# Optimization experiments

Hardware: AMD Instinct MI355X
Metric: run time of the kernel (lower is better)

The kernel has to match this reference:

```python
import jax, jax.numpy as jnp
import numpy as np

B, N, T, F, H, O = 32, 256, 64, 16, 128, 1  # batch, nodes, seq_len, input, hidden, output


def setup_inputs() -> dict:
    key = jax.random.key(0)
    ks = jax.random.split(key, 14)
    s = 0.05
    nrm = lambda k, shp: jax.random.normal(k, shp, jnp.float32) * s
    return {
        "x": jax.random.normal(ks[0], (B, N, T, F), jnp.float32),
        "A": jax.random.normal(ks[1], (N, N), jnp.float32),
        "W_ih0": nrm(ks[2], (4 * H, F)),
        "W_hh0": nrm(ks[3], (4 * H, H)),
        "b_ih0": nrm(ks[4], (4 * H,)),
        "b_hh0": nrm(ks[5], (4 * H,)),
        "W_ih1": nrm(ks[6], (4 * H, H)),
        "W_hh1": nrm(ks[7], (4 * H, H)),
        "b_ih1": nrm(ks[8], (4 * H,)),
        "b_hh1": nrm(ks[9], (4 * H,)),
        "W1": nrm(ks[10], (H, H)),
        "W2": nrm(ks[11], (H, H)),
        "W3": nrm(ks[12], (H, H)),
        "Wfc": nrm(ks[13], (O, H)),
    }


def _lstm_layer(inp, W_ih, W_hh, b_ih, b_hh):
    # inp: (BN, T, F_in). PyTorch LSTM gate order: i, f, g, o.
    BN = inp.shape[0]
    Hd = W_hh.shape[1]
    h0 = jnp.zeros((BN, Hd), inp.dtype)
    c0 = jnp.zeros((BN, Hd), inp.dtype)

    def step(carry, x_t):
        h, c = carry
        g = x_t @ W_ih.T + b_ih + h @ W_hh.T + b_hh
        i, f, gg, o = jnp.split(g, 4, axis=-1)
        c = jax.nn.sigmoid(f) * c + jax.nn.sigmoid(i) * jnp.tanh(gg)
        h = jax.nn.sigmoid(o) * jnp.tanh(c)
        return (h, c), h

    (hT, _), hs = jax.lax.scan(step, (h0, c0), jnp.swapaxes(inp, 0, 1))
    return jnp.swapaxes(hs, 0, 1), hT  # (BN, T, H), (BN, H)


def reference(x, A, W_ih0, W_hh0, b_ih0, b_hh0, W_ih1, W_hh1, b_ih1, b_hh1, W1, W2, W3, Wfc):
    Bx, Nx, Tx, Fx = x.shape
    # Batch the per-node LSTM calls: all (batch, node) pairs share LSTM weights.
    xs = x.reshape(Bx * Nx, Tx, Fx)
    h1_seq, _ = _lstm_layer(xs, W_ih0, W_hh0, b_ih0, b_hh0)
    _, hT = _lstm_layer(h1_seq, W_ih1, W_hh1, b_ih1, b_hh1)  # last layer final hidden
    h_LSTM = hT.reshape(Bx, Nx, -1).transpose(0, 2, 1)  # (B, H, N)

    A_p = jax.nn.sigmoid(A)
    HA = jnp.einsum('bhn,nl->bhl', h_LSTM, A_p)        # H @ A'
    h_A = HA.transpose(0, 2, 1)                        # (B, N, H)
    W1hA = jnp.einsum('bnh,gh->bgn', h_A, W1)          # (B, H, N)
    mid = jax.nn.relu(jnp.einsum('bnh,gh->bng', h_A, W2))
    W3r = jnp.einsum('bng,fg->bfn', mid, W3)           # (B, H, N)
    ATW = jnp.einsum('bhn,nl->bhl', W3r, A_p)
    alpha = 0.9
    h_out = (1.0 - alpha) * ATW + alpha * W1hA         # (B, H, N)
    # Per-node MLP (shared weights) + sigmoid, batched over nodes.
    out = jax.nn.sigmoid(jnp.einsum('bhn,oh->bno', h_out, Wfc))  # (B, N, O)
    return out
```

## Files before the change

### kernel.cpp

```cpp
#include <hip/hip_runtime.h>


typedef __attribute__((ext_vector_type(4))) float f32x4;
typedef __attribute__((ext_vector_type(16))) float f32x16;
typedef __attribute__((ext_vector_type(2))) float f32x2;
typedef __attribute__((ext_vector_type(8))) __bf16 bf16x8;
typedef __attribute__((ext_vector_type(8))) unsigned short u16x8;
typedef __attribute__((ext_vector_type(4))) unsigned short u16x4;

#define DEV static __device__ __forceinline__

DEV unsigned short f2bf(float f) {
  unsigned u = __builtin_bit_cast(unsigned, f);
  u = u + 0x7fffu + ((u >> 16) & 1u);
  return (unsigned short)(u >> 16);
}
DEV float bf2f(unsigned short s) {
  unsigned u = ((unsigned)s) << 16;
  return __builtin_bit_cast(float, u);
}

DEV float fexp2(float x) { return __builtin_amdgcn_exp2f(x); }
DEV f32x2 exp2v2(f32x2 x) { f32x2 r; r[0] = fexp2(x[0]); r[1] = fexp2(x[1]); return r; }
DEV f32x2 rcpv2(f32x2 x) {
  f32x2 r; r[0] = __builtin_amdgcn_rcpf(x[0]); r[1] = __builtin_amdgcn_rcpf(x[1]); return r;
}

DEV unsigned cell_pair(f32x2 gi, f32x2 gf, f32x2 gg, f32x2 go, f32x2& cs) {
  const float K2 = 2.88539008f;
  f32x2 one = {1.f, 1.f};
  f32x2 t1 = exp2v2(gg);
  f32x2 t2 = exp2v2((f32x2){-gi[0], -gi[1]});
  f32x2 ef = exp2v2((f32x2){-gf[0], -gf[1]});
  f32x2 d1 = t1 + one;
  f32x2 den1 = d1 * t2 + d1;
  f32x2 it = (t1 - one) * rcpv2(den1);
  cs = rcpv2(one + ef) * cs + (f32x2){K2 * it[0], K2 * it[1]};
  f32x2 t3 = exp2v2(cs);
  f32x2 t4 = exp2v2((f32x2){-go[0], -go[1]});
  f32x2 d3 = t3 + one;
  f32x2 den3 = d3 * t4 + d3;
  f32x2 h = (t3 - one) * rcpv2(den3);
  unsigned r;
  asm("v_cvt_pk_bf16_f32 %0, %1, %2" : "=v"(r) : "v"(h[0]), "v"(h[1]));
  return r;
}

#define O_W0PK   0
#define O_W1PK   163840
#define O_APK    425984
#define O_W1APK  557056
#define O_W2APK  589824
#define O_W3APK  622592
#define O_BIAS0  655360
#define O_BIAS1  657408
#define O_HTT    659456
#define O_HAT    2756608
#define O_MIDT   4853760
#define O_W1HAT  6950912
#define O_W3R    9048064
#define O_XPK    11145216
#define O_H1     44699648

#define PREP_TOT 328704

__global__ void prep_kernel(const float* __restrict__ A,
    const float* __restrict__ Wih0, const float* __restrict__ Whh0,
    const float* __restrict__ bih0, const float* __restrict__ bhh0,
    const float* __restrict__ Wih1, const float* __restrict__ Whh1,
    const float* __restrict__ bih1, const float* __restrict__ bhh1,
    const float* __restrict__ W1, const float* __restrict__ W2,
    const float* __restrict__ W3, char* __restrict__ ws)
{
  const float K1 = 1.44269504f, K2 = 2.88539008f;
  int idx = blockIdx.x * blockDim.x + threadIdx.x;
  if (idx >= PREP_TOT) return;
  if (idx < 81920) {
    int o = idx, i = o & 7, l = (o >> 3) & 63, f = o >> 9;
    int kt = f % 10, W = f / 10;
    int rho = l & 31, hik = l >> 5;
    int p = rho & 3, hi = (rho >> 2) & 1, q = rho >> 3;
    int gc = p * 128 + 8 * W + 4 * hi + q;
    float sc = (p == 2) ? K2 : K1;
    int k = 16 * kt + 8 * hik + i;
    float v;
    if (k < 128) v = Whh0[gc * 128 + k];
    else {
      int kk = k - 128;
      v = (kk < 16) ? Wih0[gc * 16 + kk]
                    : (kk == 16 ? (bih0[gc] + bhh0[gc]) : 0.f);
    }
    ((unsigned short*)(ws + O_W0PK))[idx] = f2bf(v * sc);
  } else if (idx < 212992) {
    int o = idx - 81920, i = o & 7, l = (o >> 3) & 63, f = o >> 9;
    int kt = f & 15, W = f >> 4;
    int rho = l & 31, hik = l >> 5;
    int p = rho & 3, hi = (rho >> 2) & 1, q = rho >> 3;
    int gc = p * 128 + 8 * W + 4 * hi + q;
    float sc = (p == 2) ? K2 : K1;
    int k = 16 * kt + 8 * hik + i;
    float v = (k < 128) ? Wih1[gc * 128 + k] : Whh1[gc * 128 + (k - 128)];
    ((unsigned short*)(ws + O_W1PK))[o] = f2bf(v * sc);
  } else if (idx < 278528) {
    int o = idx - 212992, i = o & 7, l = (o >> 3) & 63, f = o >> 9;
    int kt = f & 7, ct = f >> 3;
    int n = 32 * kt + 8 * (l >> 4) + i;
    int lc = 16 * ct + (l & 15);
    float e = fexp2(-K1 * A[n * 256 + lc]);
    ((unsigned short*)(ws + O_APK))[o] = f2bf(__builtin_amdgcn_rcpf(1.f + e));
  } else if (idx < 327680) {
    int o = idx - 278528;
    int m = o >> 14;
    int oo = o & 16383;
    int i = oo & 7, l = (oo >> 3) & 63, f = oo >> 9;
    int kt = f & 3, rt = f >> 2;
    int g = 16 * rt + (l & 15);
    int k = 32 * kt + 8 * (l >> 4) + i;
    const float* W = (m == 0) ? W1 : (m == 1) ? W2 : W3;
    unsigned short* dst = (unsigned short*)(ws + ((m == 0) ? O_W1APK : (m == 1) ? O_W2APK : O_W3APK));
    dst[oo] = f2bf(W[g * 128 + k]);
  } else if (idx < 328192) {
    int c = idx - 327680;
    ((float*)(ws + O_BIAS0))[c] = bih0[c] + bhh0[c];
  } else {
    int c = idx - 328192;
    float sc = ((c >> 7) == 2) ? K2 : K1;
    ((float*)(ws + O_BIAS1))[c] = (bih1[c] + bhh1[c]) * sc;
  }
}

__global__ void prepx_kernel(const float* __restrict__ x, char* __restrict__ ws)
{
  int tid = blockIdx.x * 256 + threadIdx.x;
  int lane = tid & 63;
  int slice = (tid >> 6) & 1;
  int t = (tid >> 7) & 63;
  int rt32 = tid >> 13;
  int col = lane & 31, hi = lane >> 5;
  u16x8 v = (u16x8)0;
  if (slice == 0) {
    const float* p = x + ((long)(rt32 * 32 + col) * 64 + t) * 16 + 8 * hi;
    float4 a = *(const float4*)p;
    float4 b = *(const float4*)(p + 4);
    v[0] = f2bf(a.x); v[1] = f2bf(a.y); v[2] = f2bf(a.z); v[3] = f2bf(a.w);
    v[4] = f2bf(b.x); v[5] = f2bf(b.y); v[6] = f2bf(b.z); v[7] = f2bf(b.w);
  } else if (hi == 0) {
    v[0] = 0x3F80;
  }
  ((u16x8*)(ws + O_XPK))[tid] = v;
}

__global__ __launch_bounds__(1024, 4) void lstm0_k(char* __restrict__ ws, int row_base)
{
  const unsigned short* W0pk = (const unsigned short*)(ws + O_W0PK);
  const unsigned short* xpk = (const unsigned short*)(ws + O_XPK);
  unsigned short* h1 = (unsigned short*)(ws + O_H1);

  int tid = threadIdx.x;
  int Wv = tid >> 6, l = tid & 63, col = l & 31, hi = l >> 5;
  int lrow = blockIdx.x * 32;
  long grow0 = (long)row_base + lrow;

  __shared__ unsigned char hlds[2][8192];
  ((unsigned long long*)hlds[0])[tid] = 0ull;

  bf16x8 Af[10];
#pragma unroll
  for (int kt = 0; kt < 10; kt++)
    Af[kt] = ((const bf16x8*)W0pk)[(Wv * 10 + kt) * 64 + l];

  f32x2 cs01 = {0.f, 0.f}, cs23 = {0.f, 0.f};

  int rd[8];
#pragma unroll
  for (int ks = 0; ks < 8; ks++)
    rd[ks] = col * 256 + ((32 * ks + 16 * hi) ^ ((col & 15) << 4));
  int whp = col * 256 + ((16 * Wv + 8 * hi) ^ ((col & 15) << 4));

  int pr = tid >> 5, pc8 = tid & 31;
  int sld = pr * 256 + ((8 * pc8) ^ ((pr & 15) << 4));
  unsigned short* st = h1 + (long)(lrow + pr) * 8192 + 4 * pc8;

  long xbase = (grow0 >> 5) * 8192 + l;
  const bf16x8* xpf = (const bf16x8*)xpk;
  bf16x8 xb0 = xpf[xbase], xb1 = xpf[xbase + 64];
  __syncthreads();

  for (int t = 0; t < 64; t++) {
    const unsigned char* rbuf = hlds[t & 1];
    unsigned char* wbuf = hlds[(t & 1) ^ 1];
    int tn = (t < 63) ? t + 1 : 63;
    bf16x8 xb0n = xpf[xbase + tn * 128];
    bf16x8 xb1n = xpf[xbase + tn * 128 + 64];

    f32x16 acc = (f32x16)0.f;
    __builtin_amdgcn_s_setprio(1);
#pragma unroll
    for (int ks = 0; ks < 8; ks++) {
      bf16x8 hb = *(const bf16x8*)(rbuf + rd[ks]);
      acc = __builtin_amdgcn_mfma_f32_32x32x16_bf16(Af[ks], hb, acc, 0, 0, 0);
    }
    acc = __builtin_amdgcn_mfma_f32_32x32x16_bf16(Af[8], xb0, acc, 0, 0, 0);
    acc = __builtin_amdgcn_mfma_f32_32x32x16_bf16(Af[9], xb1, acc, 0, 0, 0);
    __builtin_amdgcn_s_setprio(0);

    unsigned pk01 = cell_pair((f32x2){acc[0], acc[4]}, (f32x2){acc[1], acc[5]},
                              (f32x2){acc[2], acc[6]}, (f32x2){acc[3], acc[7]}, cs01);
    unsigned pk23 = cell_pair((f32x2){acc[8], acc[12]}, (f32x2){acc[9], acc[13]},
                              (f32x2){acc[10], acc[14]}, (f32x2){acc[11], acc[15]}, cs23);
    *(unsigned long long*)(wbuf + whp) =
        ((unsigned long long)pk23 << 32) | pk01;
    xb0 = xb0n; xb1 = xb1n;
    __syncthreads();
    *(unsigned long long*)(st + t * 128) =
        *(const unsigned long long*)(hlds[(t & 1) ^ 1] + sld);
  }
}

__global__ __launch_bounds__(1024, 4) void lstm1_k(char* __restrict__ ws, int row_base)
{
  const unsigned short* W1pk = (const unsigned short*)(ws + O_W1PK);
  const float* bias1 = (const float*)(ws + O_BIAS1);
  const unsigned short* h1 = (const unsigned short*)(ws + O_H1);
  unsigned short* hTt = (unsigned short*)(ws + O_HTT);

  int tid = threadIdx.x;
  int Wv = tid >> 6, l = tid & 63, col = l & 31, hi = l >> 5;
  int lrow = blockIdx.x * 32;
  long grow0 = (long)row_base + lrow;

  __shared__ unsigned char hlds[2][8192];
  __shared__ unsigned char h1s[2][8192];
  ((unsigned long long*)hlds[0])[tid] = 0ull;

  int prow = tid >> 5, pc8 = tid & 31;
  const unsigned short* s0 = h1 + (long)(lrow + prow) * 8192 + 4 * pc8;
  int d0 = prow * 256 + ((8 * pc8) ^ ((prow & 15) << 4));
  *(unsigned long long*)(h1s[0] + d0) = *(const unsigned long long*)s0;

  bf16x8 Af[16];
#pragma unroll
  for (int kt = 0; kt < 16; kt++)
    Af[kt] = ((const bf16x8*)W1pk)[(Wv * 16 + kt) * 64 + l];

  int u0 = 8 * Wv + 4 * hi;
  f32x16 bias_c;
#pragma unroll
  for (int r = 0; r < 16; r++)
    bias_c[r] = bias1[(r & 3) * 128 + u0 + (r >> 2)];

  f32x2 cs01 = {0.f, 0.f}, cs23 = {0.f, 0.f};

  int rd[8];
#pragma unroll
  for (int ks = 0; ks < 8; ks++)
    rd[ks] = col * 256 + ((32 * ks + 16 * hi) ^ ((col & 15) << 4));
  int whp = col * 256 + ((16 * Wv + 8 * hi) ^ ((col & 15) << 4));
  __syncthreads();

  for (int t = 0; t < 64; t++) {
    const unsigned char* rbuf = hlds[t & 1];
    unsigned char* wbuf = hlds[(t & 1) ^ 1];
    const unsigned char* h1r = h1s[t & 1];
    unsigned char* h1w = h1s[(t & 1) ^ 1];
    int tn = (t < 63) ? t + 1 : 63;
    unsigned long long pf = *(const unsigned long long*)(s0 + tn * 128);

    f32x16 acc = bias_c;
    __builtin_amdgcn_s_setprio(1);
#pragma unroll
    for (int ks = 0; ks < 8; ks++) {
      bf16x8 xb = *(const bf16x8*)(h1r + rd[ks]);
      acc = __builtin_amdgcn_mfma_f32_32x32x16_bf16(Af[ks], xb, acc, 0, 0, 0);
    }
#pragma unroll
    for (int ks = 0; ks < 8; ks++) {
      bf16x8 hb = *(const bf16x8*)(rbuf + rd[ks]);
      acc = __builtin_amdgcn_mfma_f32_32x32x16_bf16(Af[8 + ks], hb, acc, 0, 0, 0);
    }
    __builtin_amdgcn_s_setprio(0);

    unsigned pk01 = cell_pair((f32x2){acc[0], acc[4]}, (f32x2){acc[1], acc[5]},
                              (f32x2){acc[2], acc[6]}, (f32x2){acc[3], acc[7]}, cs01);
    unsigned pk23 = cell_pair((f32x2){acc[8], acc[12]}, (f32x2){acc[9], acc[13]},
                              (f32x2){acc[10], acc[14]}, (f32x2){acc[11], acc[15]}, cs23);
    *(unsigned long long*)(wbuf + whp) =
        ((unsigned long long)pk23 << 32) | pk01;
    *(unsigned long long*)(h1w + d0) = pf;
    __syncthreads();
  }

  {
    unsigned long long hp = *(const unsigned long long*)(hlds[0] + whp);
    long grow = grow0 + col;
    long base = ((grow >> 8) * 128) * 256 + (grow & 255);
#pragma unroll
    for (int j = 0; j < 4; j++)
      hTt[base + (long)(u0 + j) * 256] = (unsigned short)((hp >> (16 * j)) & 0xffff);
  }
}

__global__ __launch_bounds__(256, 2) void g1_kernel(char* __restrict__ ws)
{
  const unsigned short* hTt = (const unsigned short*)(ws + O_HTT);
  const unsigned short* Apk = (const unsigned short*)(ws + O_APK);
  unsigned short* HAt = (unsigned short*)(ws + O_HAT);
  int tid = threadIdx.x, w = tid >> 6, l = tid & 63, lr = l & 15, lq = l >> 4;
  int bi = blockIdx.x;
  int b = bi >> 3, rtp = (bi >> 1) & 3, ch = bi & 1;
  f32x4 acc[2][2];
#pragma unroll
  for (int i = 0; i < 2; i++)
#pragma unroll
    for (int j = 0; j < 2; j++) acc[i][j] = (f32x4){0.f, 0.f, 0.f, 0.f};
  for (int kt = 0; kt < 8; kt++) {
    bf16x8 af[2];
#pragma unroll
    for (int rtl = 0; rtl < 2; rtl++) {
      int rt = rtp * 2 + rtl;
      af[rtl] = *(const bf16x8*)(hTt + (long)(b * 128 + 16 * rt + lr) * 256 + 32 * kt + 8 * lq);
    }
#pragma unroll
    for (int cti = 0; cti < 2; cti++) {
      int ct = w * 4 + ch * 2 + cti;
      bf16x8 bf = ((const bf16x8*)Apk)[(ct * 8 + kt) * 64 + l];
#pragma unroll
      for (int rtl = 0; rtl < 2; rtl++)
        acc[rtl][cti] = __builtin_amdgcn_mfma_f32_16x16x32_bf16(af[rtl], bf, acc[rtl][cti], 0, 0, 0);
    }
  }
#pragma unroll
  for (int rtl = 0; rtl < 2; rtl++)
#pragma unroll
    for (int cti = 0; cti < 2; cti++) {
      int rt = rtp * 2 + rtl, ct = w * 4 + ch * 2 + cti;
      u16x4 pk;
#pragma unroll
      for (int r = 0; r < 4; r++) pk[r] = f2bf(acc[rtl][cti][r]);
      *(u16x4*)(HAt + (long)(b * 256 + 16 * ct + lr) * 128 + 16 * rt + 4 * lq) = pk;
    }
}

__global__ __launch_bounds__(256, 2) void g2_kernel(char* __restrict__ ws)
{
  const unsigned short* HAt = (const unsigned short*)(ws + O_HAT);
  const unsigned short* W1apk = (const unsigned short*)(ws + O_W1APK);
  const unsigned short* W2apk = (const unsigned short*)(ws + O_W2APK);
  unsigned short* W1hAt = (unsigned short*)(ws + O_W1HAT);
  unsigned short* midT = (unsigned short*)(ws + O_MIDT);
  int tid = threadIdx.x, w = tid >> 6, l = tid & 63, lr = l & 15, lq = l >> 4;
  int bi = blockIdx.x;
  int b = bi >> 3, rtp = (bi >> 1) & 3, ch = bi & 1;
  f32x4 a1[2][2], a2[2][2];
#pragma unroll
  for (int i = 0; i < 2; i++)
#pragma unroll
    for (int j = 0; j < 2; j++) { a1[i][j] = (f32x4){0.f,0.f,0.f,0.f}; a2[i][j] = (f32x4){0.f,0.f,0.f,0.f}; }
  for (int kt = 0; kt < 4; kt++) {
    bf16x8 af1[2], af2[2];
#pragma unroll
    for (int rtl = 0; rtl < 2; rtl++) {
      int rt = rtp * 2 + rtl;
      af1[rtl] = ((const bf16x8*)W1apk)[(rt * 4 + kt) * 64 + l];
      af2[rtl] = ((const bf16x8*)W2apk)[(rt * 4 + kt) * 64 + l];
    }
#pragma unroll
    for (int cti = 0; cti < 2; cti++) {
      int ct = w * 4 + ch * 2 + cti;
      bf16x8 bf = *(const bf16x8*)(HAt + (long)(b * 256 + 16 * ct + lr) * 128 + 32 * kt + 8 * lq);
#pragma unroll
      for (int rtl = 0; rtl < 2; rtl++) {
        a1[rtl][cti] = __builtin_amdgcn_mfma_f32_16x16x32_bf16(af1[rtl], bf, a1[rtl][cti], 0, 0, 0);
        a2[rtl][cti] = __builtin_amdgcn_mfma_f32_16x16x32_bf16(af2[rtl], bf, a2[rtl][cti], 0, 0, 0);
      }
    }
  }
#pragma unroll
  for (int rtl = 0; rtl < 2; rtl++)
#pragma unroll
    for (int cti = 0; cti < 2; cti++) {
      int rt = rtp * 2 + rtl, ct = w * 4 + ch * 2 + cti;
      u16x4 p1, p2;
#pragma unroll
      for (int r = 0; r < 4; r++) {
        p1[r] = f2bf(a1[rtl][cti][r]);
        p2[r] = f2bf(fmaxf(a2[rtl][cti][r], 0.f));
      }
      long off = (long)(b * 256 + 16 * ct + lr) * 128 + 16 * rt + 4 * lq;
      *(u16x4*)(W1hAt + off) = p1;
      *(u16x4*)(midT + off) = p2;
    }
}

__global__ __launch_bounds__(256, 2) void g3_kernel(char* __restrict__ ws)
{
  const unsigned short* midT = (const unsigned short*)(ws + O_MIDT);
  const unsigned short* W3apk = (const unsigned short*)(ws + O_W3APK);
  unsigned short* W3r = (unsigned short*)(ws + O_W3R);
  int tid = threadIdx.x, w = tid >> 6, l = tid & 63, lr = l & 15, lq = l >> 4;
  int bi = blockIdx.x;
  int b = bi >> 3, rtp = (bi >> 1) & 3, ch = bi & 1;
  f32x4 acc[2][2];
#pragma unroll
  for (int i = 0; i < 2; i++)
#pragma unroll
    for (int j = 0; j < 2; j++) acc[i][j] = (f32x4){0.f, 0.f, 0.f, 0.f};
  for (int kt = 0; kt < 4; kt++) {
    bf16x8 af[2];
#pragma unroll
    for (int rtl = 0; rtl < 2; rtl++)
      af[rtl] = ((const bf16x8*)W3apk)[((rtp * 2 + rtl) * 4 + kt) * 64 + l];
#pragma unroll
    for (int cti = 0; cti < 2; cti++) {
      int ct = w * 4 + ch * 2 + cti;
      bf16x8 bf = *(const bf16x8*)(midT + (long)(b * 256 + 16 * ct + lr) * 128 + 32 * kt + 8 * lq);
#pragma unroll
      for (int rtl = 0; rtl < 2; rtl++)
        acc[rtl][cti] = __builtin_amdgcn_mfma_f32_16x16x32_bf16(af[rtl], bf, acc[rtl][cti], 0, 0, 0);
    }
  }
#pragma unroll
  for (int rtl = 0; rtl < 2; rtl++)
#pragma unroll
    for (int cti = 0; cti < 2; cti++) {
      int rt = rtp * 2 + rtl, ct = w * 4 + ch * 2 + cti;
#pragma unroll
      for (int r = 0; r < 4; r++)
        W3r[(long)(b * 128 + 16 * rt + 4 * lq + r) * 256 + 16 * ct + lr] = f2bf(acc[rtl][cti][r]);
    }
}

__global__ __launch_bounds__(256, 2) void g4_kernel(char* __restrict__ ws,
    const float* __restrict__ Wfc, float* __restrict__ out)
{
  const unsigned short* W3r = (const unsigned short*)(ws + O_W3R);
  const unsigned short* Apk = (const unsigned short*)(ws + O_APK);
  const unsigned short* W1hAt = (const unsigned short*)(ws + O_W1HAT);
  int tid = threadIdx.x, w = tid >> 6, l = tid & 63, lr = l & 15, lq = l >> 4;
  int bi = blockIdx.x;
  int b = bi >> 2, cq = bi & 3;
  int ct = cq * 4 + w;
  f32x4 acc[8];
#pragma unroll
  for (int i = 0; i < 8; i++) acc[i] = (f32x4){0.f, 0.f, 0.f, 0.f};
  for (int kt = 0; kt < 8; kt++) {
    bf16x8 bfv = ((const bf16x8*)Apk)[(ct * 8 + kt) * 64 + l];
#pragma unroll
    for (int rt = 0; rt < 8; rt++) {
      bf16x8 af = *(const bf16x8*)(W3r + (long)(b * 128 + 16 * rt + lr) * 256 + 32 * kt + 8 * lq);
      acc[rt] = __builtin_amdgcn_mfma_f32_16x16x32_bf16(af, bfv, acc[rt], 0, 0, 0);
    }
  }
  float psum = 0.f;
#pragma unroll
  for (int rt = 0; rt < 8; rt++) {
    float4 wf = *(const float4*)(Wfc + 16 * rt + 4 * lq);
    u16x4 wv = *(const u16x4*)(W1hAt + (long)(b * 256 + 16 * ct + lr) * 128 + 16 * rt + 4 * lq);
    psum += wf.x * (0.1f * acc[rt][0] + 0.9f * bf2f(wv[0]));
    psum += wf.y * (0.1f * acc[rt][1] + 0.9f * bf2f(wv[1]));
    psum += wf.z * (0.1f * acc[rt][2] + 0.9f * bf2f(wv[2]));
    psum += wf.w * (0.1f * acc[rt][3] + 0.9f * bf2f(wv[3]));
  }
  psum += __shfl_xor(psum, 16);
  psum += __shfl_xor(psum, 32);
  if (lq == 0) out[b * 256 + ct * 16 + lr] = __builtin_amdgcn_rcpf(1.f + fexp2(-1.44269504f * psum));
}

extern "C" void kernel_launch(void* const* d_in, const int* in_sizes, int n_in,
                              void* d_out, int out_size, void* d_ws, size_t ws_size,
                              hipStream_t stream)
{
  const float* x    = (const float*)d_in[0];
  const float* A    = (const float*)d_in[1];
  const float* Wih0 = (const float*)d_in[2];
  const float* Whh0 = (const float*)d_in[3];
  const float* bih0 = (const float*)d_in[4];
  const float* bhh0 = (const float*)d_in[5];
  const float* Wih1 = (const float*)d_in[6];
  const float* Whh1 = (const float*)d_in[7];
  const float* bih1 = (const float*)d_in[8];
  const float* bhh1 = (const float*)d_in[9];
  const float* W1   = (const float*)d_in[10];
  const float* W2   = (const float*)d_in[11];
  const float* W3   = (const float*)d_in[12];
  const float* Wfc  = (const float*)d_in[13];
  char* ws = (char*)d_ws;

  prep_kernel<<<(PREP_TOT + 255) / 256, 256, 0, stream>>>(
      A, Wih0, Whh0, bih0, bhh0, Wih1, Whh1, bih1, bhh1, W1, W2, W3, ws);
  prepx_kernel<<<8192, 256, 0, stream>>>(x, ws);

  size_t need_full = (size_t)O_H1 + 134217728u;
  size_t need_half = (size_t)O_H1 + 67108864u;
  if (ws_size >= need_full) {
    lstm0_k<<<256, 1024, 0, stream>>>(ws, 0);
    lstm1_k<<<256, 1024, 0, stream>>>(ws, 0);
  } else if (ws_size >= need_half) {
    for (int c = 0; c < 2; c++) {
      lstm0_k<<<128, 1024, 0, stream>>>(ws, c * 4096);
      lstm1_k<<<128, 1024, 0, stream>>>(ws, c * 4096);
    }
  } else {
    for (int c = 0; c < 4; c++) {
      lstm0_k<<<64, 1024, 0, stream>>>(ws, c * 2048);
      lstm1_k<<<64, 1024, 0, stream>>>(ws, c * 2048);
    }
  }

  g1_kernel<<<256, 256, 0, stream>>>(ws);
  g2_kernel<<<256, 256, 0, stream>>>(ws);
  g3_kernel<<<256, 256, 0, stream>>>(ws);
  g4_kernel<<<128, 256, 0, stream>>>(ws, Wfc, (float*)d_out);
}
```

Baseline: 274.2 us.

## Split LSTM gate accumulators, prefetch h1 two steps ahead, use lighter LDS barrier

Both LSTM kernels now split the gate GEMM into two independent MFMA accumulator chains (input and recurrent) that are summed before the cell update. In layer 0 the input-projection MFMAs are issued first, so they do not depend on the recurrent state loaded from LDS. Layer 1 prefetches the global h1 slice two timesteps ahead instead of one to hide more global latency. __syncthreads is replaced by a custom barrier that waits only on lgkmcnt before s_barrier, so outstanding global loads are not drained at each step. The cost is extra registers and 16 extra adds per step, which may lower occupancy.

```diff
diff --git a/kernel.cpp b/kernel.cpp
--- a/kernel.cpp
+++ b/kernel.cpp
@@ -24,6 +24,13 @@
 DEV f32x2 exp2v2(f32x2 x) { f32x2 r; r[0] = fexp2(x[0]); r[1] = fexp2(x[1]); return r; }
 DEV f32x2 rcpv2(f32x2 x) {
   f32x2 r; r[0] = __builtin_amdgcn_rcpf(x[0]); r[1] = __builtin_amdgcn_rcpf(x[1]); return r;
+}
+
+DEV void lds_barrier() {
+  asm volatile("s_waitcnt lgkmcnt(0)" ::: "memory");
+  __builtin_amdgcn_sched_barrier(0);
+  __builtin_amdgcn_s_barrier();
+  __builtin_amdgcn_sched_barrier(0);
 }
 
 DEV unsigned cell_pair(f32x2 gi, f32x2 gf, f32x2 gg, f32x2 go, f32x2& cs) {
@@ -193,16 +200,18 @@
     bf16x8 xb0n = xpf[xbase + tn * 128];
     bf16x8 xb1n = xpf[xbase + tn * 128 + 64];
 
-    f32x16 acc = (f32x16)0.f;
+    f32x16 accX = (f32x16)0.f;
+    f32x16 accH = (f32x16)0.f;
     __builtin_amdgcn_s_setprio(1);
+    accX = __builtin_amdgcn_mfma_f32_32x32x16_bf16(Af[8], xb0, accX, 0, 0, 0);
+    accX = __builtin_amdgcn_mfma_f32_32x32x16_bf16(Af[9], xb1, accX, 0, 0, 0);
 #pragma unroll
     for (int ks = 0; ks < 8; ks++) {
       bf16x8 hb = *(const bf16x8*)(rbuf + rd[ks]);
-      acc = __builtin_amdgcn_mfma_f32_32x32x16_bf16(Af[ks], hb, acc, 0, 0, 0);
-    }
-    acc = __builtin_amdgcn_mfma_f32_32x32x16_bf16(Af[8], xb0, acc, 0, 0, 0);
-    acc = __builtin_amdgcn_mfma_f32_32x32x16_bf16(Af[9], xb1, acc, 0, 0, 0);
+      accH = __builtin_amdgcn_mfma_f32_32x32x16_bf16(Af[ks], hb, accH, 0, 0, 0);
+    }
     __builtin_amdgcn_s_setprio(0);
+    f32x16 acc = accX + accH;
 
     unsigned pk01 = cell_pair((f32x2){acc[0], acc[4]}, (f32x2){acc[1], acc[5]},
                               (f32x2){acc[2], acc[6]}, (f32x2){acc[3], acc[7]}, cs01);
@@ -211,7 +220,7 @@
     *(unsigned long long*)(wbuf + whp) =
         ((unsigned long long)pk23 << 32) | pk01;
     xb0 = xb0n; xb1 = xb1n;
-    __syncthreads();
+    lds_barrier();
     *(unsigned long long*)(st + t * 128) =
         *(const unsigned long long*)(hlds[(t & 1) ^ 1] + sld);
   }
@@ -237,6 +246,7 @@
   const unsigned short* s0 = h1 + (long)(lrow + prow) * 8192 + 4 * pc8;
   int d0 = prow * 256 + ((8 * pc8) ^ ((prow & 15) << 4));
   *(unsigned long long*)(h1s[0] + d0) = *(const unsigned long long*)s0;
+  unsigned long long pf1 = *(const unsigned long long*)(s0 + 128);
 
   bf16x8 Af[16];
 #pragma unroll
@@ -263,22 +273,24 @@
     unsigned char* wbuf = hlds[(t & 1) ^ 1];
     const unsigned char* h1r = h1s[t & 1];
     unsigned char* h1w = h1s[(t & 1) ^ 1];
-    int tn = (t < 63) ? t + 1 : 63;
-    unsigned long long pf = *(const unsigned long long*)(s0 + tn * 128);
-
-    f32x16 acc = bias_c;
+    int t2 = (t < 62) ? t + 2 : 63;
+    unsigned long long pf2 = *(const unsigned long long*)(s0 + t2 * 128);
+
+    f32x16 accI = bias_c;
+    f32x16 accR = (f32x16)0.f;
     __builtin_amdgcn_s_setprio(1);
 #pragma unroll
     for (int ks = 0; ks < 8; ks++) {
       bf16x8 xb = *(const bf16x8*)(h1r + rd[ks]);
-      acc = __builtin_amdgcn_mfma_f32_32x32x16_bf16(Af[ks], xb, acc, 0, 0, 0);
+      accI = __builtin_amdgcn_mfma_f32_32x32x16_bf16(Af[ks], xb, accI, 0, 0, 0);
     }
 #pragma unroll
     for (int ks = 0; ks < 8; ks++) {
       bf16x8 hb = *(const bf16x8*)(rbuf + rd[ks]);
-      acc = __builtin_amdgcn_mfma_f32_32x32x16_bf16(Af[8 + ks], hb, acc, 0, 0, 0);
+      accR = __builtin_amdgcn_mfma_f32_32x32x16_bf16(Af[8 + ks], hb, accR, 0, 0, 0);
     }
     __builtin_amdgcn_s_setprio(0);
+    f32x16 acc = accI + accR;
 
     unsigned pk01 = cell_pair((f32x2){acc[0], acc[4]}, (f32x2){acc[1], acc[5]},
                               (f32x2){acc[2], acc[6]}, (f32x2){acc[3], acc[7]}, cs01);
@@ -286,8 +298,9 @@
                               (f32x2){acc[10], acc[14]}, (f32x2){acc[11], acc[15]}, cs23);
     *(unsigned long long*)(wbuf + whp) =
         ((unsigned long long)pk23 << 32) | pk01;
-    *(unsigned long long*)(h1w + d0) = pf;
-    __syncthreads();
+    *(unsigned long long*)(h1w + d0) = pf1;
+    pf1 = pf2;
+    lds_barrier();
   }
 
   {
```

Result: slower. 325.7 us (+18.8%).
